# Performance work log

Measured on AMD Instinct MI355X. Metric: run time of the kernel, lower is better.

## Reference

```python
import jax, jax.numpy as jnp
import numpy as np

DIM = 512
HEADS = 8
DIM_HEAD = 64
INNER = HEADS * DIM_HEAD          # 512
CPB_DIM = DIM // 2                # 256 (ContinuousPositionBias hidden dim)
FF_INNER = int(DIM * 4 * 2 / 3)   # 1365 (GEGLU inner dim)
B, C, F, H, W = 2, 512, 8, 32, 32
SCALE = DIM_HEAD ** -0.5


def setup_inputs() -> dict:
    key = jax.random.key(0)
    ks = jax.random.split(key, 24)
    def rnd(k, shape, s=0.02):
        return jax.random.normal(k, shape, jnp.float32) * s
    return {
        "x": jax.random.normal(ks[0], (B, C, F, W, W), jnp.float32)[:, :, :, :H, :],
        # spatial attention
        "sa_gamma": jnp.ones((DIM,), jnp.float32),
        "sa_wq": rnd(ks[1], (DIM, INNER)),
        "sa_wkv": rnd(ks[2], (DIM, 2 * INNER)),
        "sa_wo": rnd(ks[3], (INNER, DIM)),
        # temporal attention
        "ta_gamma": jnp.ones((DIM,), jnp.float32),
        "ta_wq": rnd(ks[4], (DIM, INNER)),
        "ta_wkv": rnd(ks[5], (DIM, 2 * INNER)),
        "ta_wo": rnd(ks[6], (INNER, DIM)),
        # spatial ContinuousPositionBias MLP (num_dims=2, layers=2)
        "sp_w1": rnd(ks[7], (2, CPB_DIM), 0.1), "sp_b1": jnp.zeros((CPB_DIM,), jnp.float32),
        "sp_w2": rnd(ks[8], (CPB_DIM, CPB_DIM), 0.05), "sp_b2": jnp.zeros((CPB_DIM,), jnp.float32),
        "sp_w3": rnd(ks[9], (CPB_DIM, HEADS), 0.05), "sp_b3": jnp.zeros((HEADS,), jnp.float32),
        # temporal ContinuousPositionBias MLP (num_dims=1)
        "tp_w1": rnd(ks[10], (1, CPB_DIM), 0.1), "tp_b1": jnp.zeros((CPB_DIM,), jnp.float32),
        "tp_w2": rnd(ks[11], (CPB_DIM, CPB_DIM), 0.05), "tp_b2": jnp.zeros((CPB_DIM,), jnp.float32),
        "tp_w3": rnd(ks[12], (CPB_DIM, HEADS), 0.05), "tp_b3": jnp.zeros((HEADS,), jnp.float32),
        # FeedForward: Conv3d 1x1 (no bias) -> GEGLU -> RMSNorm -> Conv3d 1x1
        "ff_win": rnd(ks[13], (DIM, 2 * FF_INNER)),
        "ff_gamma": jnp.ones((FF_INNER,), jnp.float32),
        "ff_wout": rnd(ks[14], (FF_INNER, DIM)),
    }


def _rms_last(x, g):
    # torch: F.normalize(x, dim=-1) * sqrt(C) * gamma
    nrm = jnp.sqrt(jnp.sum(x * x, axis=-1, keepdims=True))
    return x / jnp.maximum(nrm, 1e-12) * jnp.sqrt(jnp.float32(x.shape[-1])) * g


def _mlp_bias(rel, w1, b1, w2, b2, w3, b3):
    h = jax.nn.silu(rel @ w1 + b1)
    h = jax.nn.silu(h @ w2 + b2)
    return h @ w3 + b3  # [R, heads]


def _cpb_2d(h, w, params):
    ry = jnp.arange(-(h - 1), h, dtype=jnp.float32)
    rx = jnp.arange(-(w - 1), w, dtype=jnp.float32)
    gy, gx = jnp.meshgrid(ry, rx, indexing='ij')
    rel = jnp.stack([gy, gx], -1).reshape(-1, 2)          # [(2h-1)(2w-1), 2]
    tab = _mlp_bias(rel, *params)                          # [R, heads]
    py, px = jnp.meshgrid(jnp.arange(h), jnp.arange(w), indexing='ij')
    pos = jnp.stack([py.reshape(-1), px.reshape(-1)], -1)  # [n, 2]
    d = pos[:, None, :] - pos[None, :, :]                  # [n, n, 2]
    idx = (d[..., 0] + h - 1) * (2 * w - 1) + (d[..., 1] + w - 1)
    return jnp.transpose(tab[idx], (2, 0, 1))              # [heads, n, n]


def _cpb_1d(f, params):
    rel = jnp.arange(-(f - 1), f, dtype=jnp.float32)[:, None]
    tab = _mlp_bias(rel, *params)                          # [2f-1, heads]
    p = jnp.arange(f)
    idx = p[:, None] - p[None, :] + f - 1
    return jnp.transpose(tab[idx], (2, 0, 1))              # [heads, f, f]


def _attn(x, gamma, wq, wkv, wo, bias):
    # x: [b, n, c]; manual softmax(QK^T*scale + bias)V (flash disabled by pos_bias)
    xn = _rms_last(x, gamma)
    q = xn @ wq
    k, v = jnp.split(xn @ wkv, 2, axis=-1)
    b, n, _ = q.shape
    rs = lambda t: t.reshape(b, n, HEADS, DIM_HEAD).transpose(0, 2, 1, 3)
    q, k, v = rs(q), rs(k), rs(v)
    s = jnp.einsum('bhid,bhjd->bhij', q, k) * SCALE + bias[None]
    a = jax.nn.softmax(s, axis=-1)
    o = jnp.einsum('bhij,bhjd->bhid', a, v)
    o = o.transpose(0, 2, 1, 3).reshape(b, n, INNER)
    return o @ wo


def _ff(x, win, gamma, wout):
    # x: [b, f, h, w, c] channel-last; Conv3d 1x1 == channel einsum
    hdn = jnp.einsum('bfhwc,co->bfhwo', x, win)
    a, gate = jnp.split(hdn, 2, axis=-1)
    y = a * jax.nn.gelu(gate, approximate=False)           # GEGLU (torch exact gelu)
    # shift_token: chunk channels, shift second half by +1 frame
    c1 = (FF_INNER + 1) // 2
    t1, t2 = y[..., :c1], y[..., c1:]
    t2 = jnp.pad(t2, ((0, 0), (1, 0), (0, 0), (0, 0), (0, 0)))[:, :-1]
    y = jnp.concatenate([t1, t2], axis=-1)
    yn = _rms_last(y, gamma)                               # RMSNorm over channels
    return jnp.einsum('bfhwi,ic->bfhwc', yn, wout)


def reference(x, sa_gamma, sa_wq, sa_wkv, sa_wo, ta_gamma, ta_wq, ta_wkv, ta_wo,
              sp_w1, sp_b1, sp_w2, sp_b2, sp_w3, sp_b3,
              tp_w1, tp_b1, tp_w2, tp_b2, tp_w3, tp_b3,
              ff_win, ff_gamma, ff_wout):
    b, c, f, h, w = x.shape
    xl = jnp.transpose(x, (0, 2, 3, 4, 1))                 # b f h w c
    # spatial attention over (h w) tokens, batched over (b f)
    xs = xl.reshape(b * f, h * w, c)
    sp_bias = _cpb_2d(h, w, (sp_w1, sp_b1, sp_w2, sp_b2, sp_w3, sp_b3))
    xs = _attn(xs, sa_gamma, sa_wq, sa_wkv, sa_wo, sp_bias) + xs
    xv = xs.reshape(b, f, h, w, c)
    # temporal attention over f tokens, batched over (b h w)
    xt = jnp.transpose(xv, (0, 2, 3, 1, 4)).reshape(b * h * w, f, c)
    tp_bias = _cpb_1d(f, (tp_w1, tp_b1, tp_w2, tp_b2, tp_w3, tp_b3))
    xt = _attn(xt, ta_gamma, ta_wq, ta_wkv, ta_wo, tp_bias) + xt
    xv = jnp.transpose(xt.reshape(b, h, w, f, c), (0, 3, 1, 2, 4))
    # GEGLU feedforward with token shift
    xv = _ff(xv, ff_win, ff_gamma, ff_wout) + xv
    return jnp.transpose(xv, (0, 4, 1, 2, 3))              # b c f h w
```

## Files before the change

kernel.cpp:

```cpp
#include <hip/hip_runtime.h>
#include <cstdint>
#include <cstddef>

typedef __bf16 bf16_t;
typedef __bf16 bf16x8 __attribute__((ext_vector_type(8)));
typedef float floatx4 __attribute__((ext_vector_type(4)));

__device__ __forceinline__ float wred_sum(float v) {
#pragma unroll
  for (int off = 32; off > 0; off >>= 1) v += __shfl_xor(v, off);
  return v;
}
__device__ __forceinline__ void async16(const void* g, void* l) {
  __builtin_amdgcn_global_load_lds((const __attribute__((address_space(1))) void*)g,
                                   (__attribute__((address_space(3))) void*)l, 16, 0, 0);
}

template <bool OUT_BF16, bool RESID>
__global__ __launch_bounds__(256) void st_gemm(
    const bf16_t* __restrict__ A, const bf16_t* __restrict__ B, void* Cp,
    const float* Res, int M, int N, int K, int lda, int ldb, int ldc, int nb1,
    long long sa1, long long sa2, long long sb1, long long sb2,
    long long sc1, long long sc2) {
  __shared__ bf16_t sA[128 * 32];
  __shared__ bf16_t sB[128 * 32];
  const int z = blockIdx.z;
  const int z1 = z % nb1, z2 = z / nb1;
  A += z1 * sa1 + z2 * sa2;
  B += z1 * sb1 + z2 * sb2;
  const long long coff = z1 * sc1 + z2 * sc2;
  const int tid = threadIdx.x;
  const int bm = blockIdx.x, bn = blockIdx.y;
  const int lane = tid & 63;
  const int wave = tid >> 6;
  const int wm = (wave >> 1) * 64, wn = (wave & 1) * 64;
  const int rowf = lane & 15, kq = (lane >> 4) * 8;

  floatx4 acc[4][4];
#pragma unroll
  for (int i = 0; i < 4; ++i)
#pragma unroll
    for (int j = 0; j < 4; ++j) acc[i][j] = floatx4{0.f, 0.f, 0.f, 0.f};

  for (int kt = 0; kt < K; kt += 32) {
#pragma unroll
    for (int it = 0; it < 2; ++it) {
      int slot = it * 256 + tid;
      int mi = slot >> 2, kc = slot & 3;
      int ar = bm * 128 + mi; if (ar > M - 1) ar = M - 1;
      int br = bn * 128 + mi; if (br > N - 1) br = N - 1;
      async16(A + (size_t)ar * lda + kt + kc * 8, (char*)sA + slot * 16);
      async16(B + (size_t)br * ldb + kt + kc * 8, (char*)sB + slot * 16);
    }
    __syncthreads();
    bf16x8 af[4], bv[4];
#pragma unroll
    for (int i = 0; i < 4; ++i) {
      af[i] = *(const bf16x8*)(sA + (wm + i * 16 + rowf) * 32 + kq);
      bv[i] = *(const bf16x8*)(sB + (wn + i * 16 + rowf) * 32 + kq);
    }
#pragma unroll
    for (int i = 0; i < 4; ++i)
#pragma unroll
      for (int j = 0; j < 4; ++j)
        acc[i][j] = __builtin_amdgcn_mfma_f32_16x16x32_bf16(af[i], bv[j], acc[i][j], 0, 0, 0);
    __syncthreads();
  }

  const int colBase = bn * 128 + wn + (lane & 15);
  const int rowBase = bm * 128 + wm + (lane >> 4) * 4;
#pragma unroll
  for (int i = 0; i < 4; ++i) {
#pragma unroll
    for (int j = 0; j < 4; ++j) {
      int col = colBase + j * 16;
      if (col >= N) continue;
#pragma unroll
      for (int r = 0; r < 4; ++r) {
        int row = rowBase + i * 16 + r;
        if (row >= M) continue;
        long long idx = coff + (long long)row * ldc + col;
        float v = acc[i][j][r];
        if (RESID) v += Res[idx];
        if (OUT_BF16) ((bf16_t*)Cp)[idx] = (bf16_t)v;
        else          ((float*)Cp)[idx] = v;
      }
    }
  }
}

__global__ __launch_bounds__(256) void st_transpose2d(
    const float* __restrict__ in, float* __restrict__ out, int R, int Cc,
    long long inb, long long outb) {
  __shared__ float tile[32][33];
  const int ct = blockIdx.x, rt = blockIdx.y, b = blockIdx.z;
  in += (long long)b * inb;
  out += (long long)b * outb;
  const int tx = threadIdx.x & 31, ty = threadIdx.x >> 5;
#pragma unroll
  for (int k = 0; k < 4; ++k) {
    int r = rt * 32 + ty + k * 8;
    int c = ct * 32 + tx;
    tile[ty + k * 8][tx] = in[(size_t)r * Cc + c];
  }
  __syncthreads();
#pragma unroll
  for (int k = 0; k < 4; ++k) {
    int c = ct * 32 + ty + k * 8;
    int r = rt * 32 + tx;
    out[(size_t)c * R + r] = tile[tx][ty + k * 8];
  }
}

__global__ void st_wtrans(const float* __restrict__ src, bf16_t* __restrict__ dst,
                          int K, int Kpad, int N, int srcld, int coloff, long total) {
  long idx = (long)blockIdx.x * 256 + threadIdx.x;
  if (idx >= total) return;
  int kp = (int)(idx % Kpad);
  int n = (int)(idx / Kpad);
  float v = (kp < K) ? src[(size_t)kp * srcld + coloff + n] : 0.f;
  dst[idx] = (bf16_t)v;
}

__global__ __launch_bounds__(256) void st_cpb(
    const float* __restrict__ w1, const float* __restrict__ b1,
    const float* __restrict__ w2, const float* __restrict__ b2,
    const float* __restrict__ w3, const float* __restrict__ b3,
    bf16_t* __restrict__ tab2d, float* __restrict__ tab1d, int two_d) {
  const int pos = blockIdx.x, t = threadIdx.x;
  float r0, r1 = 0.f;
  if (two_d) { r0 = (float)(pos / 63 - 31); r1 = (float)(pos % 63 - 31); }
  else { r0 = (float)(pos - 7); }
  __shared__ float sh[256];
  float h = r0 * w1[t] + (two_d ? r1 * w1[256 + t] : 0.f) + b1[t];
  h = h / (1.f + expf(-h));
  sh[t] = h;
  __syncthreads();
  float h2 = b2[t];
  for (int j = 0; j < 256; ++j) h2 += sh[j] * w2[j * 256 + t];
  h2 = h2 / (1.f + expf(-h2));
  __syncthreads();
  sh[t] = h2;
  __syncthreads();
  if (t < 8) {
    float o = b3[t];
    for (int j = 0; j < 256; ++j) o += sh[j] * w3[j * 8 + t];
    if (two_d) tab2d[t * 4000 + pos] = (bf16_t)o;
    else tab1d[t * 15 + pos] = o;
  }
}

__global__ __launch_bounds__(256) void st_rmsnorm(const float* __restrict__ x,
                                                  const float* __restrict__ gamma,
                                                  bf16_t* __restrict__ y) {
  const int token = blockIdx.x * 4 + (threadIdx.x >> 6);
  const int lane = threadIdx.x & 63;
  const float* xr = x + (size_t)token * 512;
  float v[8];
  float ss = 0.f;
#pragma unroll
  for (int k = 0; k < 8; ++k) { v[k] = xr[k * 64 + lane]; ss += v[k] * v[k]; }
  ss = wred_sum(ss);
  const float r = 22.627416998f / fmaxf(sqrtf(ss), 1e-12f);
  bf16_t* yr = y + (size_t)token * 512;
#pragma unroll
  for (int k = 0; k < 8; ++k) yr[k * 64 + lane] = (bf16_t)(v[k] * r * gamma[k * 64 + lane]);
}

__global__ void st_cast(const float* __restrict__ in, bf16_t* __restrict__ out, long n) {
  long i = (long)blockIdx.x * 256 + threadIdx.x;
  if (i < n) out[i] = (bf16_t)in[i];
}

__global__ __launch_bounds__(256) void st_vtrans(const bf16_t* __restrict__ qkv,
                                                 bf16_t* __restrict__ vT) {
  __shared__ float tile[32][33];
  const int jt = blockIdx.x, dt = blockIdx.y, z = blockIdx.z;
  const int bf = z >> 3, h = z & 7;
  const int tx = threadIdx.x & 31, ty = threadIdx.x >> 5;
#pragma unroll
  for (int k = 0; k < 4; ++k) {
    int j = jt * 32 + ty + k * 8;
    int d = dt * 32 + tx;
    tile[ty + k * 8][tx] = (float)qkv[((size_t)(bf * 1024 + j)) * 1536 + 1024 + h * 64 + d];
  }
  __syncthreads();
#pragma unroll
  for (int k = 0; k < 4; ++k) {
    int d = dt * 32 + ty + k * 8;
    int j = jt * 32 + tx;
    vT[((size_t)z * 64 + d) * 1024 + j] = (bf16_t)tile[tx][ty + k * 8];
  }
}

__global__ __launch_bounds__(256) void st_flash(
    const bf16_t* __restrict__ qkv, const bf16_t* __restrict__ vT,
    const bf16_t* __restrict__ tabb, bf16_t* __restrict__ ob) {
  __shared__ bf16_t ldsQ[128 * 64];
  __shared__ bf16_t ldsK[64 * 64];
  __shared__ bf16_t ldsV[64 * 64];
  __shared__ bf16_t ldsP[4 * 32 * 72];
  __shared__ bf16_t ldsT[4000];
  const int qtile = blockIdx.x;
  const int z = blockIdx.y;
  const int bf = z >> 3, h = z & 7;
  const int tid = threadIdx.x;
  const int lane = tid & 63, wave = tid >> 6;
  const int cl = lane & 15, g = lane >> 4;
  const size_t qkvBase = (size_t)bf * 1024 * 1536 + h * 64;
#pragma unroll
  for (int it = 0; it < 4; ++it) {
    int slot = it * 256 + tid;
    int row = slot >> 3, c = slot & 7;
    int cs = c ^ (row & 7);
    async16(qkv + qkvBase + (size_t)(qtile * 128 + row) * 1536 + cs * 8,
            (char*)ldsQ + slot * 16);
  }
#pragma unroll
  for (int it = 0; it < 2; ++it) {
    int slot = it * 256 + tid;
    if (slot < 500)
      async16(tabb + h * 4000 + slot * 8, (char*)ldsT + slot * 16);
  }
  int fi[2][4];
#pragma unroll
  for (int it = 0; it < 2; ++it)
#pragma unroll
    for (int r = 0; r < 4; ++r) {
      int i = qtile * 128 + wave * 32 + it * 16 + g * 4 + r;
      fi[it][r] = (i >> 5) * 63 + (i & 31) + 1984;
    }
  float lsum[2][4];
  floatx4 oacc[2][4];
#pragma unroll
  for (int it = 0; it < 2; ++it)
#pragma unroll
    for (int r = 0; r < 4; ++r) lsum[it][r] = 0.f;
#pragma unroll
  for (int it = 0; it < 2; ++it)
#pragma unroll
    for (int dt = 0; dt < 4; ++dt) oacc[it][dt] = floatx4{0.f, 0.f, 0.f, 0.f};

  bf16_t* ldsPw = ldsP + wave * (32 * 72);
  const size_t vBase = (size_t)z * 64 * 1024;

  for (int j0 = 0; j0 < 1024; j0 += 64) {
#pragma unroll
    for (int it = 0; it < 2; ++it) {
      int slot = it * 256 + tid;
      int row = slot >> 3, c = slot & 7;
      int cs = c ^ (row & 7);
      async16(qkv + qkvBase + 512 + (size_t)(j0 + row) * 1536 + cs * 8,
              (char*)ldsK + slot * 16);
      async16(vT + vBase + (size_t)row * 1024 + j0 + cs * 8,
              (char*)ldsV + slot * 16);
    }
    __syncthreads();
    floatx4 sacc[2][4];
#pragma unroll
    for (int it = 0; it < 2; ++it)
#pragma unroll
      for (int jt = 0; jt < 4; ++jt) sacc[it][jt] = floatx4{0.f, 0.f, 0.f, 0.f};
#pragma unroll
    for (int ks = 0; ks < 2; ++ks) {
      bf16x8 aq[2];
#pragma unroll
      for (int it = 0; it < 2; ++it) {
        int row = wave * 32 + it * 16 + cl;
        int cs = (g + ks * 4) ^ (row & 7);
        aq[it] = *(const bf16x8*)(ldsQ + row * 64 + cs * 8);
      }
#pragma unroll
      for (int jt = 0; jt < 4; ++jt) {
        int col = jt * 16 + cl;
        int cs = (g + ks * 4) ^ (col & 7);
        bf16x8 bk = *(const bf16x8*)(ldsK + col * 64 + cs * 8);
#pragma unroll
        for (int it = 0; it < 2; ++it)
          sacc[it][jt] = __builtin_amdgcn_mfma_f32_16x16x32_bf16(aq[it], bk, sacc[it][jt], 0, 0, 0);
      }
    }
#pragma unroll
    for (int jt = 0; jt < 4; ++jt) {
      int j = j0 + jt * 16 + cl;
      int fj = (j >> 5) * 63 + (j & 31);
#pragma unroll
      for (int it = 0; it < 2; ++it) {
#pragma unroll
        for (int r = 0; r < 4; ++r) {
          float e = __expf(sacc[it][jt][r] * 0.125f + (float)ldsT[fi[it][r] - fj]);
          lsum[it][r] += e;
          ldsPw[(it * 16 + g * 4 + r) * 72 + jt * 16 + cl] = (bf16_t)e;
        }
      }
    }
#pragma unroll
    for (int ks = 0; ks < 2; ++ks) {
      bf16x8 ap[2];
#pragma unroll
      for (int it = 0; it < 2; ++it)
        ap[it] = *(const bf16x8*)(ldsPw + (it * 16 + cl) * 72 + (g + ks * 4) * 8);
#pragma unroll
      for (int dt = 0; dt < 4; ++dt) {
        int d = dt * 16 + cl;
        int cs = (g + ks * 4) ^ (d & 7);
        bf16x8 bv = *(const bf16x8*)(ldsV + d * 64 + cs * 8);
#pragma unroll
        for (int it = 0; it < 2; ++it)
          oacc[it][dt] = __builtin_amdgcn_mfma_f32_16x16x32_bf16(ap[it], bv, oacc[it][dt], 0, 0, 0);
      }
    }
    __syncthreads();
  }
#pragma unroll
  for (int it = 0; it < 2; ++it)
#pragma unroll
    for (int r = 0; r < 4; ++r) {
#pragma unroll
      for (int x = 1; x < 16; x <<= 1) lsum[it][r] += __shfl_xor(lsum[it][r], x);
      lsum[it][r] = 1.f / lsum[it][r];
    }
#pragma unroll
  for (int it = 0; it < 2; ++it) {
#pragma unroll
    for (int r = 0; r < 4; ++r) {
      int i = qtile * 128 + wave * 32 + it * 16 + g * 4 + r;
      size_t base = ((size_t)bf * 1024 + i) * 512 + h * 64;
#pragma unroll
      for (int dt = 0; dt < 4; ++dt)
        ob[base + dt * 16 + cl] = (bf16_t)(oacc[it][dt][r] * lsum[it][r]);
    }
  }
}

__global__ __launch_bounds__(256) void st_tattn2(const bf16_t* __restrict__ qkv,
                                                 const float* __restrict__ tabf,
                                                 bf16_t* __restrict__ o) {
  const int wg = blockIdx.x * 4 + (threadIdx.x >> 6);
  const int bhw = wg >> 3, head = wg & 7;
  const int lane = threadIdx.x & 63;
  const size_t base = (size_t)bhw * 8 * 1536 + head * 64 + lane;
  float q[8], k[8], v[8];
#pragma unroll
  for (int f = 0; f < 8; ++f) {
    q[f] = (float)qkv[base + (size_t)f * 1536];
    k[f] = (float)qkv[base + (size_t)f * 1536 + 512];
    v[f] = (float)qkv[base + (size_t)f * 1536 + 1024];
  }
  float p[64];
#pragma unroll
  for (int i = 0; i < 8; ++i)
#pragma unroll
    for (int j = 0; j < 8; ++j) p[i * 8 + j] = q[i] * k[j];
#pragma unroll
  for (int st = 32; st >= 1; st >>= 1) {
    const bool hi = (lane & st) != 0;
#pragma unroll
    for (int m = 0; m < st; ++m) {
      float give = hi ? p[m] : p[m + st];
      float keep = hi ? p[m + st] : p[m];
      p[m] = keep + __shfl_xor(give, st);
    }
  }
  const int i = lane >> 3, j = lane & 7;
  float e = __expf(p[0] * 0.125f + tabf[head * 15 + i - j + 7]);
  float sm = e;
  sm += __shfl_xor(sm, 1);
  sm += __shfl_xor(sm, 2);
  sm += __shfl_xor(sm, 4);
  const float prob = e / sm;
  float acc[8];
#pragma unroll
  for (int ii = 0; ii < 8; ++ii) acc[ii] = 0.f;
#pragma unroll
  for (int ii = 0; ii < 8; ++ii)
#pragma unroll
    for (int jj = 0; jj < 8; ++jj)
      acc[ii] += __shfl(prob, ii * 8 + jj) * v[jj];
#pragma unroll
  for (int ii = 0; ii < 8; ++ii)
    o[(size_t)(bhw * 8 + ii) * 512 + head * 64 + lane] = (bf16_t)acc[ii];
}

__global__ void st_permute(const float* __restrict__ in, float* __restrict__ out, int dir) {
  size_t idx = (size_t)blockIdx.x * 256 + threadIdx.x;
  int c = (int)(idx & 511);
  size_t r = idx >> 9;
  size_t src;
  if (dir == 0) {
    int f = (int)(r & 7);
    int hw = (int)((r >> 3) & 1023);
    int b = (int)(r >> 13);
    src = ((((size_t)b * 8 + f) * 1024 + hw) << 9) + c;
  } else {
    int hw = (int)(r & 1023);
    int f = (int)((r >> 10) & 7);
    int b = (int)(r >> 13);
    src = ((((size_t)b * 1024 + hw) * 8 + f) << 9) + c;
  }
  out[idx] = in[src];
}

__global__ __launch_bounds__(256) void st_glu(const bf16_t* __restrict__ a,
                                              const bf16_t* __restrict__ g,
                                              const float* __restrict__ gamma,
                                              bf16_t* __restrict__ yn) {
  const int t = blockIdx.x;
  const int tid = threadIdx.x;
  const int f = (t >> 10) & 7;
  float y[6];
  float ss = 0.f;
#pragma unroll
  for (int kk = 0; kk < 6; ++kk) {
    int c = kk * 256 + tid;
    float yv = 0.f;
    if (c < 1365) {
      long src = t;
      bool valid = true;
      if (c >= 683) { if (f == 0) valid = false; else src = t - 1024; }
      if (valid) {
        float av = (float)a[src * 1365 + c];
        float gv = (float)g[src * 1365 + c];
        yv = av * 0.5f * gv * (1.f + erff(gv * 0.70710678f));
      }
    }
    y[kk] = yv;
    ss += yv * yv;
  }
  __shared__ float red[4];
  ss = wred_sum(ss);
  if ((tid & 63) == 0) red[tid >> 6] = ss;
  __syncthreads();
  ss = red[0] + red[1] + red[2] + red[3];
  const float r = sqrtf(1365.f) / fmaxf(sqrtf(ss), 1e-12f);
#pragma unroll
  for (int kk = 0; kk < 6; ++kk) {
    int c = kk * 256 + tid;
    if (c < 1365) yn[(size_t)t * 1376 + c] = (bf16_t)(y[kk] * r * gamma[c]);
  }
  if (tid < 11) yn[(size_t)t * 1376 + 1365 + tid] = (bf16_t)0.f;
}

extern "C" void kernel_launch(void* const* d_in, const int* in_sizes, int n_in,
                              void* d_out, int out_size, void* d_ws, size_t ws_size,
                              hipStream_t stream) {
  const float* x        = (const float*)d_in[0];
  const float* sa_gamma = (const float*)d_in[1];
  const float* sa_wq    = (const float*)d_in[2];
  const float* sa_wkv   = (const float*)d_in[3];
  const float* sa_wo    = (const float*)d_in[4];
  const float* ta_gamma = (const float*)d_in[5];
  const float* ta_wq    = (const float*)d_in[6];
  const float* ta_wkv   = (const float*)d_in[7];
  const float* ta_wo    = (const float*)d_in[8];
  const float* sp_w1 = (const float*)d_in[9];
  const float* sp_b1 = (const float*)d_in[10];
  const float* sp_w2 = (const float*)d_in[11];
  const float* sp_b2 = (const float*)d_in[12];
  const float* sp_w3 = (const float*)d_in[13];
  const float* sp_b3 = (const float*)d_in[14];
  const float* tp_w1 = (const float*)d_in[15];
  const float* tp_b1 = (const float*)d_in[16];
  const float* tp_w2 = (const float*)d_in[17];
  const float* tp_b2 = (const float*)d_in[18];
  const float* tp_w3 = (const float*)d_in[19];
  const float* tp_b3 = (const float*)d_in[20];
  const float* ff_win   = (const float*)d_in[21];
  const float* ff_gamma = (const float*)d_in[22];
  const float* ff_wout  = (const float*)d_in[23];
  float* outp = (float*)d_out;

  char* ws = (char*)d_ws;
  size_t off = 0;
  auto alloc = [&](size_t bytes) -> char* {
    char* p = ws + off;
    off += (bytes + 255) & ~(size_t)255;
    return p;
  };
  const long T = 16384;
  float*  xs  = (float*)alloc((size_t)T * 512 * 4);
  bf16_t* xn  = (bf16_t*)alloc((size_t)T * 512 * 2);
  char*   R2  = alloc((size_t)T * 1536 * 2);
  char*   R3  = alloc((size_t)T * 1536 * 2);
  bf16_t* ynb = (bf16_t*)alloc((size_t)T * 1376 * 2);
  bf16_t* wqkvT_sa = (bf16_t*)alloc(1536ULL * 512 * 2);
  bf16_t* woT_sa   = (bf16_t*)alloc(512ULL * 512 * 2);
  bf16_t* wqkvT_ta = (bf16_t*)alloc(1536ULL * 512 * 2);
  bf16_t* woT_ta   = (bf16_t*)alloc(512ULL * 512 * 2);
  bf16_t* winAT = (bf16_t*)alloc(1365ULL * 512 * 2);
  bf16_t* winGT = (bf16_t*)alloc(1365ULL * 512 * 2);
  bf16_t* woutT = (bf16_t*)alloc(512ULL * 1376 * 2);
  bf16_t* tabb  = (bf16_t*)alloc(8 * 4000 * 2);
  float*  tabf  = (float*)alloc(8 * 15 * 4);

  bf16_t* qkv  = (bf16_t*)R2;
  bf16_t* abuf = (bf16_t*)R2;
  bf16_t* vT   = (bf16_t*)R3;
  bf16_t* ob_s = (bf16_t*)(R3 + (size_t)T * 512 * 2);
  float*  xt   = (float*)R3;
  bf16_t* ob_t = (bf16_t*)(R3 + (size_t)T * 512 * 4);
  bf16_t* gbuf = (bf16_t*)R3;

  st_transpose2d<<<dim3(256, 16, 2), 256, 0, stream>>>(x, xs, 512, 8192,
                                                       (long long)512 * 8192, (long long)512 * 8192);
  auto wt = [&](const float* src, bf16_t* dst, int K, int Kpad, int N, int srcld, int coloff) {
    long tot = (long)N * Kpad;
    st_wtrans<<<dim3((tot + 255) / 256), 256, 0, stream>>>(src, dst, K, Kpad, N, srcld, coloff, tot);
  };
  wt(sa_wq, wqkvT_sa, 512, 512, 512, 512, 0);
  wt(sa_wkv, wqkvT_sa + 512 * 512, 512, 512, 1024, 1024, 0);
  wt(sa_wo, woT_sa, 512, 512, 512, 512, 0);
  wt(ta_wq, wqkvT_ta, 512, 512, 512, 512, 0);
  wt(ta_wkv, wqkvT_ta + 512 * 512, 512, 512, 1024, 1024, 0);
  wt(ta_wo, woT_ta, 512, 512, 512, 512, 0);
  wt(ff_win, winAT, 512, 512, 1365, 2730, 0);
  wt(ff_win, winGT, 512, 512, 1365, 2730, 1365);
  wt(ff_wout, woutT, 1365, 1376, 512, 512, 0);
  st_cpb<<<dim3(3969), 256, 0, stream>>>(sp_w1, sp_b1, sp_w2, sp_b2, sp_w3, sp_b3, tabb, tabf, 1);
  st_cpb<<<dim3(15), 256, 0, stream>>>(tp_w1, tp_b1, tp_w2, tp_b2, tp_w3, tp_b3, tabb, tabf, 0);

  st_rmsnorm<<<dim3(4096), 256, 0, stream>>>(xs, sa_gamma, xn);
  st_gemm<true, false><<<dim3(128, 12, 1), 256, 0, stream>>>(
      xn, wqkvT_sa, (void*)qkv, nullptr, 16384, 1536, 512, 512, 512, 1536, 1, 0, 0, 0, 0, 0, 0);
  st_vtrans<<<dim3(32, 2, 128), 256, 0, stream>>>(qkv, vT);
  st_flash<<<dim3(8, 128), 256, 0, stream>>>(qkv, vT, tabb, ob_s);
  st_gemm<false, true><<<dim3(128, 4, 1), 256, 0, stream>>>(
      ob_s, woT_sa, (void*)xs, xs, 16384, 512, 512, 512, 512, 512, 1, 0, 0, 0, 0, 0, 0);

  st_permute<<<dim3(32768), 256, 0, stream>>>(xs, xt, 0);
  st_rmsnorm<<<dim3(4096), 256, 0, stream>>>(xt, ta_gamma, xn);
  st_gemm<true, false><<<dim3(128, 12, 1), 256, 0, stream>>>(
      xn, wqkvT_ta, (void*)qkv, nullptr, 16384, 1536, 512, 512, 512, 1536, 1, 0, 0, 0, 0, 0, 0);
  st_tattn2<<<dim3(4096), 256, 0, stream>>>(qkv, tabf, ob_t);
  st_gemm<false, true><<<dim3(128, 4, 1), 256, 0, stream>>>(
      ob_t, woT_ta, (void*)xt, xt, 16384, 512, 512, 512, 512, 512, 1, 0, 0, 0, 0, 0, 0);
  st_permute<<<dim3(32768), 256, 0, stream>>>(xt, xs, 1);

  st_cast<<<dim3(32768), 256, 0, stream>>>(xs, xn, T * 512);
  st_gemm<true, false><<<dim3(128, 11, 1), 256, 0, stream>>>(
      xn, winAT, (void*)abuf, nullptr, 16384, 1365, 512, 512, 512, 1365, 1, 0, 0, 0, 0, 0, 0);
  st_gemm<true, false><<<dim3(128, 11, 1), 256, 0, stream>>>(
      xn, winGT, (void*)gbuf, nullptr, 16384, 1365, 512, 512, 512, 1365, 1, 0, 0, 0, 0, 0, 0);
  st_glu<<<dim3(16384), 256, 0, stream>>>(abuf, gbuf, ff_gamma, ynb);
  st_gemm<false, true><<<dim3(128, 4, 1), 256, 0, stream>>>(
      ynb, woutT, (void*)xs, xs, 16384, 512, 1376, 1376, 1376, 512, 1, 0, 0, 0, 0, 0, 0);

  st_transpose2d<<<dim3(16, 256, 2), 256, 0, stream>>>(xs, outp, 8192, 512,
                                                       (long long)8192 * 512, (long long)8192 * 512);
}
```

Baseline: 779.2 us.

## Restructure flash LDS use, fuse FF input GEMMs, fold cast into permute

The spatial flash kernel now keeps Q fragments in registers instead of staging them in LDS, loads only the slice of the bias table each query tile needs, and swizzles the P buffer instead of padding it. Together with a launch-bounds hint of 4 blocks per CU, this cuts LDS use so more blocks can be resident. In the feedforward, the separate value and gate input GEMMs are merged into one GEMM over the concatenated weight with a single interleaved output buffer, and the bf16 cast is folded into the preceding permute kernel. This removes a kernel launch and a full extra read of activations, at the cost of more register pressure in flash and a wider output row in the GLU reads.

Result: slower. 839.8 us (+7.8%).

```diff
diff --git a/kernel.cpp b/kernel.cpp
--- a/kernel.cpp
+++ b/kernel.cpp
@@ -167,11 +167,6 @@
   for (int k = 0; k < 8; ++k) yr[k * 64 + lane] = (bf16_t)(v[k] * r * gamma[k * 64 + lane]);
 }
 
-__global__ void st_cast(const float* __restrict__ in, bf16_t* __restrict__ out, long n) {
-  long i = (long)blockIdx.x * 256 + threadIdx.x;
-  if (i < n) out[i] = (bf16_t)in[i];
-}
-
 __global__ __launch_bounds__(256) void st_vtrans(const bf16_t* __restrict__ qkv,
                                                  bf16_t* __restrict__ vT) {
   __shared__ float tile[32][33];
@@ -193,14 +188,13 @@
   }
 }
 
-__global__ __launch_bounds__(256) void st_flash(
+__global__ __launch_bounds__(256, 4) void st_flash(
     const bf16_t* __restrict__ qkv, const bf16_t* __restrict__ vT,
     const bf16_t* __restrict__ tabb, bf16_t* __restrict__ ob) {
-  __shared__ bf16_t ldsQ[128 * 64];
-  __shared__ bf16_t ldsK[64 * 64];
-  __shared__ bf16_t ldsV[64 * 64];
-  __shared__ bf16_t ldsP[4 * 32 * 72];
-  __shared__ bf16_t ldsT[4000];
+  __shared__ __align__(16) bf16_t ldsK[64 * 64];
+  __shared__ __align__(16) bf16_t ldsV[64 * 64];
+  __shared__ __align__(16) bf16_t ldsP[4 * 32 * 64];
+  __shared__ __align__(16) bf16_t ldsT[2216];
   const int qtile = blockIdx.x;
   const int z = blockIdx.y;
   const int bf = z >> 3, h = z & 7;
@@ -208,27 +202,29 @@
   const int lane = tid & 63, wave = tid >> 6;
   const int cl = lane & 15, g = lane >> 4;
   const size_t qkvBase = (size_t)bf * 1024 * 1536 + h * 64;
-#pragma unroll
-  for (int it = 0; it < 4; ++it) {
-    int slot = it * 256 + tid;
-    int row = slot >> 3, c = slot & 7;
-    int cs = c ^ (row & 7);
-    async16(qkv + qkvBase + (size_t)(qtile * 128 + row) * 1536 + cs * 8,
-            (char*)ldsQ + slot * 16);
-  }
+  const int eoff = (qtile * 252) & ~7;
+
 #pragma unroll
   for (int it = 0; it < 2; ++it) {
     int slot = it * 256 + tid;
-    if (slot < 500)
-      async16(tabb + h * 4000 + slot * 8, (char*)ldsT + slot * 16);
-  }
-  int fi[2][4];
+    if (slot < 277)
+      async16(tabb + h * 4000 + eoff + slot * 8, (char*)ldsT + slot * 16);
+  }
+  bf16x8 aq[2][2];
+#pragma unroll
+  for (int it = 0; it < 2; ++it)
+#pragma unroll
+    for (int ks = 0; ks < 2; ++ks) {
+      int row = qtile * 128 + wave * 32 + it * 16 + cl;
+      aq[it][ks] = *(const bf16x8*)(qkv + qkvBase + (size_t)row * 1536 + (g + ks * 4) * 8);
+    }
+  int fiB[2][4];
 #pragma unroll
   for (int it = 0; it < 2; ++it)
 #pragma unroll
     for (int r = 0; r < 4; ++r) {
       int i = qtile * 128 + wave * 32 + it * 16 + g * 4 + r;
-      fi[it][r] = (i >> 5) * 63 + (i & 31) + 1984;
+      fiB[it][r] = (i >> 5) * 63 + (i & 31) + 1984 - eoff;
     }
   float lsum[2][4];
   floatx4 oacc[2][4];
@@ -241,7 +237,7 @@
 #pragma unroll
     for (int dt = 0; dt < 4; ++dt) oacc[it][dt] = floatx4{0.f, 0.f, 0.f, 0.f};
 
-  bf16_t* ldsPw = ldsP + wave * (32 * 72);
+  bf16_t* ldsPw = ldsP + wave * (32 * 64);
   const size_t vBase = (size_t)z * 64 * 1024;
 
   for (int j0 = 0; j0 < 1024; j0 += 64) {
@@ -263,34 +259,28 @@
       for (int jt = 0; jt < 4; ++jt) sacc[it][jt] = floatx4{0.f, 0.f, 0.f, 0.f};
 #pragma unroll
     for (int ks = 0; ks < 2; ++ks) {
-      bf16x8 aq[2];
-#pragma unroll
-      for (int it = 0; it < 2; ++it) {
-        int row = wave * 32 + it * 16 + cl;
-        int cs = (g + ks * 4) ^ (row & 7);
-        aq[it] = *(const bf16x8*)(ldsQ + row * 64 + cs * 8);
-      }
 #pragma unroll
       for (int jt = 0; jt < 4; ++jt) {
         int col = jt * 16 + cl;
-        int cs = (g + ks * 4) ^ (col & 7);
-        bf16x8 bk = *(const bf16x8*)(ldsK + col * 64 + cs * 8);
+        bf16x8 bk = *(const bf16x8*)(ldsK + col * 64 + ((g + ks * 4) ^ (cl & 7)) * 8);
 #pragma unroll
         for (int it = 0; it < 2; ++it)
-          sacc[it][jt] = __builtin_amdgcn_mfma_f32_16x16x32_bf16(aq[it], bk, sacc[it][jt], 0, 0, 0);
+          sacc[it][jt] = __builtin_amdgcn_mfma_f32_16x16x32_bf16(aq[it][ks], bk, sacc[it][jt], 0, 0, 0);
       }
     }
 #pragma unroll
     for (int jt = 0; jt < 4; ++jt) {
       int j = j0 + jt * 16 + cl;
       int fj = (j >> 5) * 63 + (j & 31);
+      int pg = (jt * 2 + (cl >> 3));
 #pragma unroll
       for (int it = 0; it < 2; ++it) {
 #pragma unroll
         for (int r = 0; r < 4; ++r) {
-          float e = __expf(sacc[it][jt][r] * 0.125f + (float)ldsT[fi[it][r] - fj]);
+          float e = __expf(sacc[it][jt][r] * 0.125f + (float)ldsT[fiB[it][r] - fj]);
           lsum[it][r] += e;
-          ldsPw[(it * 16 + g * 4 + r) * 72 + jt * 16 + cl] = (bf16_t)e;
+          int prow = it * 16 + g * 4 + r;
+          ldsPw[prow * 64 + (pg ^ (prow & 7)) * 8 + (cl & 7)] = (bf16_t)e;
         }
       }
     }
@@ -299,12 +289,11 @@
       bf16x8 ap[2];
 #pragma unroll
       for (int it = 0; it < 2; ++it)
-        ap[it] = *(const bf16x8*)(ldsPw + (it * 16 + cl) * 72 + (g + ks * 4) * 8);
+        ap[it] = *(const bf16x8*)(ldsPw + (it * 16 + cl) * 64 + ((g + ks * 4) ^ (cl & 7)) * 8);
 #pragma unroll
       for (int dt = 0; dt < 4; ++dt) {
         int d = dt * 16 + cl;
-        int cs = (g + ks * 4) ^ (d & 7);
-        bf16x8 bv = *(const bf16x8*)(ldsV + d * 64 + cs * 8);
+        bf16x8 bv = *(const bf16x8*)(ldsV + d * 64 + ((g + ks * 4) ^ (cl & 7)) * 8);
 #pragma unroll
         for (int it = 0; it < 2; ++it)
           oacc[it][dt] = __builtin_amdgcn_mfma_f32_16x16x32_bf16(ap[it], bv, oacc[it][dt], 0, 0, 0);
@@ -382,7 +371,8 @@
     o[(size_t)(bhw * 8 + ii) * 512 + head * 64 + lane] = (bf16_t)acc[ii];
 }
 
-__global__ void st_permute(const float* __restrict__ in, float* __restrict__ out, int dir) {
+__global__ void st_permute(const float* __restrict__ in, float* __restrict__ out, int dir,
+                           bf16_t* __restrict__ out2) {
   size_t idx = (size_t)blockIdx.x * 256 + threadIdx.x;
   int c = (int)(idx & 511);
   size_t r = idx >> 9;
@@ -398,11 +388,12 @@
     int b = (int)(r >> 13);
     src = ((((size_t)b * 1024 + hw) * 8 + f) << 9) + c;
   }
-  out[idx] = in[src];
-}
-
-__global__ __launch_bounds__(256) void st_glu(const bf16_t* __restrict__ a,
-                                              const bf16_t* __restrict__ g,
+  float v = in[src];
+  out[idx] = v;
+  if (out2) out2[idx] = (bf16_t)v;
+}
+
+__global__ __launch_bounds__(256) void st_glu(const bf16_t* __restrict__ hdn,
                                               const float* __restrict__ gamma,
                                               bf16_t* __restrict__ yn) {
   const int t = blockIdx.x;
@@ -419,8 +410,8 @@
       bool valid = true;
       if (c >= 683) { if (f == 0) valid = false; else src = t - 1024; }
       if (valid) {
-        float av = (float)a[src * 1365 + c];
-        float gv = (float)g[src * 1365 + c];
+        float av = (float)hdn[src * 2730 + c];
+        float gv = (float)hdn[src * 2730 + 1365 + c];
         yv = av * 0.5f * gv * (1.f + erff(gv * 0.70710678f));
       }
     }
@@ -487,19 +478,17 @@
   bf16_t* woT_sa   = (bf16_t*)alloc(512ULL * 512 * 2);
   bf16_t* wqkvT_ta = (bf16_t*)alloc(1536ULL * 512 * 2);
   bf16_t* woT_ta   = (bf16_t*)alloc(512ULL * 512 * 2);
-  bf16_t* winAT = (bf16_t*)alloc(1365ULL * 512 * 2);
-  bf16_t* winGT = (bf16_t*)alloc(1365ULL * 512 * 2);
+  bf16_t* winT  = (bf16_t*)alloc(2730ULL * 512 * 2);
   bf16_t* woutT = (bf16_t*)alloc(512ULL * 1376 * 2);
   bf16_t* tabb  = (bf16_t*)alloc(8 * 4000 * 2);
   float*  tabf  = (float*)alloc(8 * 15 * 4);
 
   bf16_t* qkv  = (bf16_t*)R2;
-  bf16_t* abuf = (bf16_t*)R2;
+  bf16_t* hdn  = (bf16_t*)R2;
   bf16_t* vT   = (bf16_t*)R3;
   bf16_t* ob_s = (bf16_t*)(R3 + (size_t)T * 512 * 2);
   float*  xt   = (float*)R3;
   bf16_t* ob_t = (bf16_t*)(R3 + (size_t)T * 512 * 4);
-  bf16_t* gbuf = (bf16_t*)R3;
 
   st_transpose2d<<<dim3(256, 16, 2), 256, 0, stream>>>(x, xs, 512, 8192,
                                                        (long long)512 * 8192, (long long)512 * 8192);
@@ -513,8 +502,7 @@
   wt(ta_wq, wqkvT_ta, 512, 512, 512, 512, 0);
   wt(ta_wkv, wqkvT_ta + 512 * 512, 512, 512, 1024, 1024, 0);
   wt(ta_wo, woT_ta, 512, 512, 512, 512, 0);
-  wt(ff_win, winAT, 512, 512, 1365, 2730, 0);
-  wt(ff_win, winGT, 512, 512, 1365, 2730, 1365);
+  wt(ff_win, winT, 512, 512, 2730, 2730, 0);
   wt(ff_wout, woutT, 1365, 1376, 512, 512, 0);
   st_cpb<<<dim3(3969), 256, 0, stream>>>(sp_w1, sp_b1, sp_w2, sp_b2, sp_w3, sp_b3, tabb, tabf, 1);
   st_cpb<<<dim3(15), 256, 0, stream>>>(tp_w1, tp_b1, tp_w2, tp_b2, tp_w3, tp_b3, tabb, tabf, 0);
@@ -527,21 +515,18 @@
   st_gemm<false, true><<<dim3(128, 4, 1), 256, 0, stream>>>(
       ob_s, woT_sa, (void*)xs, xs, 16384, 512, 512, 512, 512, 512, 1, 0, 0, 0, 0, 0, 0);
 
-  st_permute<<<dim3(32768), 256, 0, stream>>>(xs, xt, 0);
+  st_permute<<<dim3(32768), 256, 0, stream>>>(xs, xt, 0, nullptr);
   st_rmsnorm<<<dim3(4096), 256, 0, stream>>>(xt, ta_gamma, xn);
   st_gemm<true, false><<<dim3(128, 12, 1), 256, 0, stream>>>(
       xn, wqkvT_ta, (void*)qkv, nullptr, 16384, 1536, 512, 512, 512, 1536, 1, 0, 0, 0, 0, 0, 0);
   st_tattn2<<<dim3(4096), 256, 0, stream>>>(qkv, tabf, ob_t);
   st_gemm<false, true><<<dim3(128, 4, 1), 256, 0, stream>>>(
       ob_t, woT_ta, (void*)xt, xt, 16384, 512, 512, 512, 512, 512, 1, 0, 0, 0, 0, 0, 0);
-  st_permute<<<dim3(32768), 256, 0, stream>>>(xt, xs, 1);
-
-  st_cast<<<dim3(32768), 256, 0, stream>>>(xs, xn, T * 512);
-  st_gemm<true, false><<<dim3(128, 11, 1), 256, 0, stream>>>(
-      xn, winAT, (void*)abuf, nullptr, 16384, 1365, 512, 512, 512, 1365, 1, 0, 0, 0, 0, 0, 0);
-  st_gemm<true, false><<<dim3(128, 11, 1), 256, 0, stream>>>(
-      xn, winGT, (void*)gbuf, nullptr, 16384, 1365, 512, 512, 512, 1365, 1, 0, 0, 0, 0, 0, 0);
-  st_glu<<<dim3(16384), 256, 0, stream>>>(abuf, gbuf, ff_gamma, ynb);
+  st_permute<<<dim3(32768), 256, 0, stream>>>(xt, xs, 1, xn);
+
+  st_gemm<true, false><<<dim3(128, 22, 1), 256, 0, stream>>>(
+      xn, winT, (void*)hdn, nullptr, 16384, 2730, 512, 512, 512, 2730, 1, 0, 0, 0, 0, 0, 0);
+  st_glu<<<dim3(16384), 256, 0, stream>>>(hdn, ff_gamma, ynb);
   st_gemm<false, true><<<dim3(128, 4, 1), 256, 0, stream>>>(
       ynb, woutT, (void*)xs, xs, 16384, 512, 1376, 1376, 1376, 512, 1, 0, 0, 0, 0, 0, 0);
 
```
